# Kernel tuning notes

Measured on AMD Instinct MI355X. Metric: run time of the kernel, lower is better.

## Reference

```python
import jax, jax.numpy as jnp
import numpy as np

IN_SIZE = 1024
CLASSES = 7
N = 50000
LN_EPS = 1e-5


def _chain(x, w, b, g, beta):
    # Linear -> (Dropout=identity at eval) -> LayerNorm -> GELU(exact erf)
    h = x @ w.T + b
    mu = jnp.mean(h, axis=-1, keepdims=True)
    var = jnp.var(h, axis=-1, keepdims=True)
    h = (h - mu) / jnp.sqrt(var + LN_EPS) * g + beta
    return jax.nn.gelu(h, approximate=False)


def setup_inputs() -> dict:
    key = jax.random.key(0)
    ks = jax.random.split(key, 16)
    d = IN_SIZE
    std = 1.0 / np.sqrt(d)
    inp = {
        "features": jax.random.normal(ks[0], (N, d), jnp.float32),
        "c": jax.random.normal(ks[1], (N, CLASSES), jnp.float32),
        "key_w": jax.random.uniform(ks[2], (d, d), jnp.float32, -std, std),
        "key_b": jax.random.uniform(ks[3], (d,), jnp.float32, -std, std),
        "key_g": jnp.ones((d,), jnp.float32),
        "key_beta": jnp.zeros((d,), jnp.float32),
        "query_w": jax.random.uniform(ks[4], (d, d), jnp.float32, -std, std),
        "query_b": jax.random.uniform(ks[5], (d,), jnp.float32, -std, std),
        "query_g": jnp.ones((d,), jnp.float32),
        "query_beta": jnp.zeros((d,), jnp.float32),
        "value_w": jax.random.uniform(ks[6], (d, d), jnp.float32, -std, std),
        "value_b": jax.random.uniform(ks[7], (d,), jnp.float32, -std, std),
        "value_g": jnp.ones((d,), jnp.float32),
        "value_beta": jnp.zeros((d,), jnp.float32),
        "head_w": jax.random.uniform(ks[8], (CLASSES, CLASSES, d), jnp.float32, -1.0 / np.sqrt(CLASSES * d), 1.0 / np.sqrt(CLASSES * d)),
        "head_b": jax.random.uniform(ks[9], (CLASSES,), jnp.float32, -1.0 / np.sqrt(CLASSES * d), 1.0 / np.sqrt(CLASSES * d)),
    }
    return inp


def reference(features, c, key_w, key_b, key_g, key_beta,
              query_w, query_b, query_g, query_beta,
              value_w, value_b, value_g, value_beta,
              head_w, head_b):
    K = _chain(features, key_w, key_b, key_g, key_beta)          # [N, d]
    V = _chain(K, value_w, value_b, value_g, value_beta)         # [N, d]
    Q = _chain(K, query_w, query_b, query_g, query_beta)         # [N, d]
    # critical (top-scoring) instance per class
    top_idx = jnp.argmax(c, axis=0)                              # [classes]
    m_feats = K[top_idx]                                         # [classes, d]
    q_max = _chain(m_feats, query_w, query_b, query_g, query_beta)  # [classes, d]
    A = Q @ q_max.T                                              # [N, classes]
    A = jax.nn.softmax(A / jnp.sqrt(jnp.float32(Q.shape[1])), axis=0)
    B = A.T @ V                                                  # [classes, d]
    # Conv1d(classes, classes, kernel_size=d) on [1, classes, d] -> full contraction
    C = jnp.einsum('ik,oik->o', B, head_w) + head_b              # [classes]
    C = C.reshape(1, -1)
    return (C, A, B.reshape(1, CLASSES, -1))
```

## Files before the change

### kernel.cpp

```cpp
#include <hip/hip_runtime.h>


typedef unsigned short u16;
typedef __attribute__((ext_vector_type(8))) short          bf16x8;
typedef __attribute__((ext_vector_type(8))) unsigned short u16x8;
typedef __attribute__((ext_vector_type(4))) unsigned short u16x4;
typedef __attribute__((ext_vector_type(4))) float          f32x4;

#define DDIM  1024
#define NROWS 50000
#define MP    50176
#define NCLS  7
#define MPD4  12544

__device__ __forceinline__ u16 f2bf(float f) {
  unsigned u = __float_as_uint(f);
  u = (u + 0x7FFFu + ((u >> 16) & 1u)) >> 16;
  return (u16)u;
}
__device__ __forceinline__ float bf2f(u16 h) {
  return __uint_as_float(((unsigned)h) << 16);
}
__device__ __forceinline__ float gelu(float x) {
  return 0.5f * x * (1.0f + erff(x * 0.70710678118654752f));
}

__device__ __forceinline__ void load16_lds(const u16* g, u16* l) {
  __builtin_amdgcn_global_load_lds(
      (const __attribute__((address_space(1))) unsigned int*)(const void*)g,
      (__attribute__((address_space(3))) unsigned int*)(void*)l, 16, 0, 0);
}

#define MFMA_(a, b, c) __builtin_amdgcn_mfma_f32_16x16x32_bf16(a, b, c, 0, 0, 0)

__global__ __launch_bounds__(256) void k_convw(const float* __restrict__ kw,
                                               const float* __restrict__ vw,
                                               const float* __restrict__ qw,
                                               u16* __restrict__ Wk,
                                               u16* __restrict__ Wvq) {
  const int w = blockIdx.x >> 7;
  const int b = blockIdx.x & 127;
  const float* src = (w == 0) ? kw : (w == 1) ? vw : qw;
  u16* dst = (w == 0) ? Wk : (Wvq + (size_t)(w - 1) * DDIM * DDIM);
  for (int i = b * 256 + threadIdx.x; i < DDIM * DDIM / 8; i += 128 * 256) {
    const float4* p = (const float4*)(src + (size_t)i * 8);
    float4 f0 = p[0], f1 = p[1];
    u16x8 o;
    o[0] = f2bf(f0.x); o[1] = f2bf(f0.y); o[2] = f2bf(f0.z); o[3] = f2bf(f0.w);
    o[4] = f2bf(f1.x); o[5] = f2bf(f1.y); o[6] = f2bf(f1.z); o[7] = f2bf(f1.w);
    *(u16x8*)(dst + (size_t)i * 8) = o;
  }
}

template<int AFP32>
__global__ __launch_bounds__(256) void k_gemm(const float* __restrict__ Af,
                                              const u16* __restrict__ Ab,
                                              const u16* __restrict__ B,
                                              u16* __restrict__ C,
                                              int lnn, int ldc) {
  __shared__ __align__(16) u16 As[128 * 32];
  __shared__ __align__(16) u16 Bs[128 * 32];
  const int tid  = threadIdx.x;
  const int lane = tid & 63;
  const int cpx = gridDim.x >> 3;
  const int v   = (blockIdx.x & 7) * cpx + (blockIdx.x >> 3);
  const int m0 = (v >> lnn) * 128;
  const int n0 = (v & ((1 << lnn) - 1)) * 128;
  const int wid = tid >> 6;
  const int wr = (wid >> 1) * 64;
  const int wc = (wid & 1) * 64;

  const int rA = tid >> 2;
  const int slotl = tid & 3;
  const int swz = (rA >> 1) & 3;
  const int cA = ((slotl ^ swz) << 3);
  const u16* Bp0 = B + (size_t)(n0 + rA) * DDIM + cA;
  const u16* Bp1 = Bp0 + (size_t)64 * DDIM;
  const u16* Ap0 = nullptr; const u16* Ap1 = nullptr;
  const float* Fp0 = nullptr; const float* Fp1 = nullptr;
  bool av0 = false, av1 = false;
  if (AFP32) {
    av0 = (m0 + rA) < NROWS;
    av1 = (m0 + rA + 64) < NROWS;
    Fp0 = Af + (size_t)(m0 + rA) * DDIM + slotl * 8;
    Fp1 = Fp0 + (size_t)64 * DDIM;
  } else {
    Ap0 = Ab + (size_t)(m0 + rA) * DDIM + cA;
    Ap1 = Ap0 + (size_t)64 * DDIM;
  }
  const int wbase = wid * 64;
  u16* AsD0 = &As[(wbase)       * 8];
  u16* AsD1 = &As[(wbase + 256) * 8];
  u16* BsD0 = &Bs[(wbase)       * 8];
  u16* BsD1 = &Bs[(wbase + 256) * 8];
  u16* AsW0 = &As[rA * 32 + cA];
  u16* AsW1 = &As[(rA + 64) * 32 + cA];

  f32x4 acc[4][4] = {};
  const int fr = lane & 15;
  const int T  = lane >> 4;

  for (int k0 = 0; k0 < DDIM; k0 += 32) {
    float4 fa0, fb0, fa1, fb1;
    if (AFP32) {
      if (av0) { fa0 = *(const float4*)(Fp0 + k0); fb0 = *(const float4*)(Fp0 + k0 + 4); }
      if (av1) { fa1 = *(const float4*)(Fp1 + k0); fb1 = *(const float4*)(Fp1 + k0 + 4); }
    }
    __syncthreads();
    if (AFP32) {
      u16x8 o0 = {0,0,0,0,0,0,0,0}, o1 = {0,0,0,0,0,0,0,0};
      if (av0) {
        o0[0]=f2bf(fa0.x); o0[1]=f2bf(fa0.y); o0[2]=f2bf(fa0.z); o0[3]=f2bf(fa0.w);
        o0[4]=f2bf(fb0.x); o0[5]=f2bf(fb0.y); o0[6]=f2bf(fb0.z); o0[7]=f2bf(fb0.w);
      }
      if (av1) {
        o1[0]=f2bf(fa1.x); o1[1]=f2bf(fa1.y); o1[2]=f2bf(fa1.z); o1[3]=f2bf(fa1.w);
        o1[4]=f2bf(fb1.x); o1[5]=f2bf(fb1.y); o1[6]=f2bf(fb1.z); o1[7]=f2bf(fb1.w);
      }
      *(u16x8*)AsW0 = o0;
      *(u16x8*)AsW1 = o1;
    } else {
      load16_lds(Ap0 + k0, AsD0);
      load16_lds(Ap1 + k0, AsD1);
    }
    load16_lds(Bp0 + k0, BsD0);
    load16_lds(Bp1 + k0, BsD1);
    __syncthreads();
    bf16x8 a[4], b[4];
#pragma unroll
    for (int i = 0; i < 4; ++i) {
      const int R = wr + i * 16 + fr;
      a[i] = *(const bf16x8*)&As[R * 32 + ((T ^ ((R >> 1) & 3)) << 3)];
    }
#pragma unroll
    for (int j = 0; j < 4; ++j) {
      const int R = wc + j * 16 + fr;
      b[j] = *(const bf16x8*)&Bs[R * 32 + ((T ^ ((R >> 1) & 3)) << 3)];
    }
#pragma unroll
    for (int i = 0; i < 4; ++i)
#pragma unroll
      for (int j = 0; j < 4; ++j)
        acc[i][j] = MFMA_(a[i], b[j], acc[i][j]);
  }

  const int orow = (lane >> 4) * 4;
  const int ocol = lane & 15;
#pragma unroll
  for (int i = 0; i < 4; ++i)
#pragma unroll
    for (int j = 0; j < 4; ++j) {
      const size_t base = (size_t)(m0 + wr + i * 16 + orow) * ldc + (n0 + wc + j * 16 + ocol);
#pragma unroll
      for (int r = 0; r < 4; ++r)
        C[base + (size_t)r * ldc] = f2bf(acc[i][j][r]);
    }
}

__global__ __launch_bounds__(512, 2) void k_gemm256(const u16* __restrict__ A,
                                                    const u16* __restrict__ Bw,
                                                    u16* __restrict__ C) {
  extern __shared__ __align__(16) u16 smem[];
  u16* Abase = smem;
  u16* Bbase = smem + 32768;
  const int tid  = threadIdx.x;
  const int lane = tid & 63;
  const int wid  = tid >> 6;
  const int wr = wid >> 2;
  const int wc = wid & 3;
  const int bh = wc >> 1;
  const int bl = (wc & 1) * 64;
  const int fr = lane & 15;
  const int T  = lane >> 4;
  const int v  = (blockIdx.x & 7) * 196 + (blockIdx.x >> 3);
  const int m0 = (v >> 3) * 256;
  const int n0 = (v & 7) * 256;

  f32x4 acc[8][4] = {};

#define STAGE_A(KT, BB) do {                                                   \
    _Pragma("unroll") for (int h_ = 0; h_ < 2; ++h_)                           \
      _Pragma("unroll") for (int l_ = 0; l_ < 2; ++l_) {                       \
        const int s_ = l_ * 512 + tid;                                         \
        const int r_ = s_ >> 3;                                                \
        const int c_ = (s_ & 7) ^ (r_ & 7);                                    \
        load16_lds(A + (size_t)(m0 + h_ * 128 + r_) * DDIM + (KT) * 64 + c_ * 8, \
                   Abase + ((BB) * 2 + h_) * 8192 + s_ * 8);                   \
      } } while (0)

#define STAGE_B(KT, BB) do {                                                   \
    _Pragma("unroll") for (int h_ = 0; h_ < 2; ++h_)                           \
      _Pragma("unroll") for (int l_ = 0; l_ < 2; ++l_) {                       \
        const int s_ = l_ * 512 + tid;                                         \
        const int r_ = s_ >> 3;                                                \
        const int c_ = (s_ & 7) ^ (r_ & 7);                                    \
        load16_lds(Bw + (size_t)(n0 + h_ * 128 + r_) * DDIM + (KT) * 64 + c_ * 8, \
                   Bbase + ((BB) * 2 + h_) * 8192 + s_ * 8);                   \
      } } while (0)

#define PHASE_A(p) do {                                                        \
    bf16x8 afr[4];                                                             \
    _Pragma("unroll") for (int ks = 0; ks < 2; ++ks)                           \
      _Pragma("unroll") for (int ii = 0; ii < 2; ++ii) {                       \
        const int R = ((p) * 2 + ii) * 16 + fr;                                \
        afr[ks * 2 + ii] = *(const bf16x8*)&Ap[R * 64 + (((ks * 4 + T) ^ (R & 7)) << 3)]; \
      }                                                                        \
    __builtin_amdgcn_s_setprio(1);                                             \
    _Pragma("unroll") for (int ks = 0; ks < 2; ++ks)                           \
      _Pragma("unroll") for (int ii = 0; ii < 2; ++ii)                         \
        _Pragma("unroll") for (int j = 0; j < 4; ++j)                          \
          acc[(p) * 2 + ii][j] = MFMA_(afr[ks * 2 + ii], bfr[ks * 4 + j],      \
                                       acc[(p) * 2 + ii][j]);                  \
    __builtin_amdgcn_s_setprio(0);                                             \
  } while (0)

#define BARP() asm volatile("s_barrier" ::: "memory")

  STAGE_A(0, 0);
  STAGE_B(0, 0);
  asm volatile("s_waitcnt vmcnt(0)\n\ts_barrier" ::: "memory");

  for (int kt = 0; kt < 16; ++kt) {
    const int b = kt & 1;
    const u16* Ap = Abase + (b * 2 + wr) * 8192;
    const u16* Bp = Bbase + (b * 2 + bh) * 8192;
    const bool st = kt < 15;
    bf16x8 bfr[8];
    if (st) STAGE_A(kt + 1, b ^ 1);
#pragma unroll
    for (int ks = 0; ks < 2; ++ks)
#pragma unroll
      for (int j = 0; j < 4; ++j) {
        const int R = bl + j * 16 + fr;
        bfr[ks * 4 + j] = *(const bf16x8*)&Bp[R * 64 + (((ks * 4 + T) ^ (R & 7)) << 3)];
      }
    PHASE_A(0);
    BARP();
    if (st) STAGE_B(kt + 1, b ^ 1);
    PHASE_A(1);
    BARP();
    PHASE_A(2);
    BARP();
    PHASE_A(3);
    if (st)
      asm volatile("s_waitcnt vmcnt(0) lgkmcnt(0)\n\ts_barrier" ::: "memory");
  }
#undef STAGE_A
#undef STAGE_B
#undef PHASE_A
#undef BARP

#pragma unroll
  for (int i = 0; i < 8; ++i)
#pragma unroll
    for (int j = 0; j < 4; ++j) {
      const size_t base = (size_t)(m0 + wr * 128 + i * 16 + T * 4) * 2048
                        + (n0 + wc * 64 + j * 16 + fr);
#pragma unroll
      for (int r = 0; r < 4; ++r)
        C[base + (size_t)r * 2048] = f2bf(acc[i][j][r]);
    }
}

__global__ __launch_bounds__(256) void k_ln_k(const u16* __restrict__ h,
                                              const float* __restrict__ bias,
                                              const float* __restrict__ g,
                                              const float* __restrict__ beta,
                                              u16* __restrict__ out) {
  const int lane = threadIdx.x & 63;
  const int row = blockIdx.x * 4 + (threadIdx.x >> 6);
  const int c0 = lane * 8;
  u16x8* op0 = (u16x8*)(out + (size_t)row * DDIM + c0);
  u16x8* op1 = (u16x8*)(out + (size_t)row * DDIM + 512 + c0);
  if (row >= NROWS) {
    u16x8 z = {0, 0, 0, 0, 0, 0, 0, 0};
    *op0 = z; *op1 = z;
    return;
  }
  u16x8 h0 = *(const u16x8*)(h + (size_t)row * DDIM + c0);
  u16x8 h1 = *(const u16x8*)(h + (size_t)row * DDIM + 512 + c0);
  float4 a0 = *(const float4*)(bias + c0), a1 = *(const float4*)(bias + c0 + 4);
  float4 a2 = *(const float4*)(bias + 512 + c0), a3 = *(const float4*)(bias + 512 + c0 + 4);
  const float ba[8] = {a0.x, a0.y, a0.z, a0.w, a1.x, a1.y, a1.z, a1.w};
  const float bb[8] = {a2.x, a2.y, a2.z, a2.w, a3.x, a3.y, a3.z, a3.w};
  float v0[8], v1[8];
  float s1 = 0.f, s2 = 0.f;
#pragma unroll
  for (int e = 0; e < 8; ++e) {
    v0[e] = bf2f(h0[e]) + ba[e];
    v1[e] = bf2f(h1[e]) + bb[e];
    s1 += v0[e] + v1[e];
    s2 += v0[e] * v0[e] + v1[e] * v1[e];
  }
#pragma unroll
  for (int m = 1; m < 64; m <<= 1) {
    s1 += __shfl_xor(s1, m, 64);
    s2 += __shfl_xor(s2, m, 64);
  }
  const float mu = s1 * (1.0f / 1024.0f);
  const float var = s2 * (1.0f / 1024.0f) - mu * mu;
  const float rs = rsqrtf(var + 1e-5f);
  float4 g0 = *(const float4*)(g + c0), g1 = *(const float4*)(g + c0 + 4);
  float4 g2 = *(const float4*)(g + 512 + c0), g3 = *(const float4*)(g + 512 + c0 + 4);
  float4 t0 = *(const float4*)(beta + c0), t1 = *(const float4*)(beta + c0 + 4);
  float4 t2 = *(const float4*)(beta + 512 + c0), t3 = *(const float4*)(beta + 512 + c0 + 4);
  const float ga[8] = {g0.x, g0.y, g0.z, g0.w, g1.x, g1.y, g1.z, g1.w};
  const float gb[8] = {g2.x, g2.y, g2.z, g2.w, g3.x, g3.y, g3.z, g3.w};
  const float ta[8] = {t0.x, t0.y, t0.z, t0.w, t1.x, t1.y, t1.z, t1.w};
  const float tb[8] = {t2.x, t2.y, t2.z, t2.w, t3.x, t3.y, t3.z, t3.w};
  u16x8 o0, o1;
#pragma unroll
  for (int e = 0; e < 8; ++e) {
    o0[e] = f2bf(gelu((v0[e] - mu) * rs * ga[e] + ta[e]));
    o1[e] = f2bf(gelu((v1[e] - mu) * rs * gb[e] + tb[e]));
  }
  *op0 = o0; *op1 = o1;
}

__global__ __launch_bounds__(64) void k_qmax2(const float* __restrict__ argv,
                                              const int* __restrict__ argi,
                                              const u16* __restrict__ hvq,
                                              const float* __restrict__ qb,
                                              const float* __restrict__ qg,
                                              const float* __restrict__ qbeta,
                                              u16* __restrict__ qm) {
  const int j = blockIdx.x;
  const int lane = threadIdx.x;
  float bv = -3.4e38f; int bi = 0x7fffffff;
  for (int p = lane; p < 128; p += 64) {
    const float v = argv[p * NCLS + j];
    const int   i = argi[p * NCLS + j];
    if (v > bv || (v == bv && i < bi)) { bv = v; bi = i; }
  }
#pragma unroll
  for (int m = 1; m < 64; m <<= 1) {
    const float ov = __shfl_xor(bv, m, 64);
    const int   oi = __shfl_xor(bi, m, 64);
    if (ov > bv || (ov == bv && oi < bi)) { bv = ov; bi = oi; }
  }
  const int row = bi;
  const int c0 = lane * 8;
  const u16* hp = hvq + (size_t)row * 2048 + DDIM;
  u16x8 h0 = *(const u16x8*)(hp + c0);
  u16x8 h1 = *(const u16x8*)(hp + 512 + c0);
  float v0[8], v1[8];
  float s1 = 0.f, s2 = 0.f;
#pragma unroll
  for (int e = 0; e < 8; ++e) {
    v0[e] = bf2f(h0[e]) + qb[c0 + e];
    v1[e] = bf2f(h1[e]) + qb[512 + c0 + e];
    s1 += v0[e] + v1[e];
    s2 += v0[e] * v0[e] + v1[e] * v1[e];
  }
#pragma unroll
  for (int m = 1; m < 64; m <<= 1) {
    s1 += __shfl_xor(s1, m, 64);
    s2 += __shfl_xor(s2, m, 64);
  }
  const float mu = s1 * (1.0f / 1024.0f);
  const float var = s2 * (1.0f / 1024.0f) - mu * mu;
  const float rs = rsqrtf(var + 1e-5f);
  u16x8 o0, o1;
#pragma unroll
  for (int e = 0; e < 8; ++e) {
    o0[e] = f2bf(gelu((v0[e] - mu) * rs * qg[c0 + e] + qbeta[c0 + e]));
    o1[e] = f2bf(gelu((v1[e] - mu) * rs * qg[512 + c0 + e] + qbeta[512 + c0 + e]));
  }
  *(u16x8*)(qm + (size_t)j * DDIM + c0) = o0;
  *(u16x8*)(qm + (size_t)j * DDIM + 512 + c0) = o1;
}

__global__ __launch_bounds__(256) void k_ln_vq(const u16* __restrict__ h,
                                               const float* __restrict__ v_b,
                                               const float* __restrict__ v_g,
                                               const float* __restrict__ v_beta,
                                               const float* __restrict__ q_b,
                                               const float* __restrict__ q_g,
                                               const float* __restrict__ q_beta,
                                               const u16* __restrict__ qm,
                                               u16* __restrict__ V,
                                               float* __restrict__ logits) {
  __shared__ __align__(16) u16 sqm[NCLS * DDIM];
  const int tid = threadIdx.x;
  const int lane = tid & 63;
  const int half = (blockIdx.x >= MPD4) ? 1 : 0;
  const int rb = half ? (blockIdx.x - MPD4) : blockIdx.x;
  const int row = rb * 4 + (tid >> 6);
  if (half) {
    for (int i = tid; i < NCLS * DDIM / 8; i += 256)
      *(u16x8*)&sqm[i * 8] = *(const u16x8*)&qm[i * 8];
    __syncthreads();
  }
  if (row >= NROWS) return;
  const float* bias = half ? q_b : v_b;
  const float* gain = half ? q_g : v_g;
  const float* bet  = half ? q_beta : v_beta;
  const int c0 = lane * 8;
  const u16* hp = h + (size_t)row * 2048 + (size_t)half * DDIM;
  u16x8 h0 = *(const u16x8*)(hp + c0);
  u16x8 h1 = *(const u16x8*)(hp + 512 + c0);
  float4 a0 = *(const float4*)(bias + c0), a1 = *(const float4*)(bias + c0 + 4);
  float4 a2 = *(const float4*)(bias + 512 + c0), a3 = *(const float4*)(bias + 512 + c0 + 4);
  const float ba[8] = {a0.x, a0.y, a0.z, a0.w, a1.x, a1.y, a1.z, a1.w};
  const float bb[8] = {a2.x, a2.y, a2.z, a2.w, a3.x, a3.y, a3.z, a3.w};
  float v0[8], v1[8];
  float s1 = 0.f, s2 = 0.f;
#pragma unroll
  for (int e = 0; e < 8; ++e) {
    v0[e] = bf2f(h0[e]) + ba[e];
    v1[e] = bf2f(h1[e]) + bb[e];
    s1 += v0[e] + v1[e];
    s2 += v0[e] * v0[e] + v1[e] * v1[e];
  }
#pragma unroll
  for (int m = 1; m < 64; m <<= 1) {
    s1 += __shfl_xor(s1, m, 64);
    s2 += __shfl_xor(s2, m, 64);
  }
  const float mu = s1 * (1.0f / 1024.0f);
  const float var = s2 * (1.0f / 1024.0f) - mu * mu;
  const float rs = rsqrtf(var + 1e-5f);
  float4 g0 = *(const float4*)(gain + c0), g1 = *(const float4*)(gain + c0 + 4);
  float4 g2 = *(const float4*)(gain + 512 + c0), g3 = *(const float4*)(gain + 512 + c0 + 4);
  float4 t0 = *(const float4*)(bet + c0), t1 = *(const float4*)(bet + c0 + 4);
  float4 t2 = *(const float4*)(bet + 512 + c0), t3 = *(const float4*)(bet + 512 + c0 + 4);
  const float ga[8] = {g0.x, g0.y, g0.z, g0.w, g1.x, g1.y, g1.z, g1.w};
  const float gb[8] = {g2.x, g2.y, g2.z, g2.w, g3.x, g3.y, g3.z, g3.w};
  const float ta[8] = {t0.x, t0.y, t0.z, t0.w, t1.x, t1.y, t1.z, t1.w};
  const float tb[8] = {t2.x, t2.y, t2.z, t2.w, t3.x, t3.y, t3.z, t3.w};
  float y0[8], y1[8];
#pragma unroll
  for (int e = 0; e < 8; ++e) {
    y0[e] = gelu((v0[e] - mu) * rs * ga[e] + ta[e]);
    y1[e] = gelu((v1[e] - mu) * rs * gb[e] + tb[e]);
  }
  if (half == 0) {
    u16x8 o0, o1;
#pragma unroll
    for (int e = 0; e < 8; ++e) { o0[e] = f2bf(y0[e]); o1[e] = f2bf(y1[e]); }
    *(u16x8*)(V + (size_t)row * DDIM + c0) = o0;
    *(u16x8*)(V + (size_t)row * DDIM + 512 + c0) = o1;
  } else {
#pragma unroll
    for (int j = 0; j < NCLS; ++j) {
      u16x8 m0 = *(const u16x8*)&sqm[j * DDIM + c0];
      u16x8 m1 = *(const u16x8*)&sqm[j * DDIM + 512 + c0];
      float p = 0.f;
#pragma unroll
      for (int e = 0; e < 8; ++e) p += y0[e] * bf2f(m0[e]) + y1[e] * bf2f(m1[e]);
#pragma unroll
      for (int m = 1; m < 64; m <<= 1) p += __shfl_xor(p, m, 64);
      if (lane == 0) logits[(size_t)row * NCLS + j] = p * 0.03125f;
    }
  }
}

__global__ __launch_bounds__(256) void k_arg1(const float* __restrict__ c,
                                              float* __restrict__ pv,
                                              int* __restrict__ pi) {
  __shared__ float sv[256 * NCLS];
  __shared__ int   si[256 * NCLS];
  const int t = threadIdx.x;
  float bv[NCLS]; int bi[NCLS];
#pragma unroll
  for (int j = 0; j < NCLS; ++j) { bv[j] = -3.4e38f; bi[j] = 0x7fffffff; }
  for (int n = blockIdx.x * 256 + t; n < NROWS; n += 128 * 256) {
#pragma unroll
    for (int j = 0; j < NCLS; ++j) {
      const float v = c[(size_t)n * NCLS + j];
      if (v > bv[j]) { bv[j] = v; bi[j] = n; }
    }
  }
#pragma unroll
  for (int j = 0; j < NCLS; ++j) { sv[t * NCLS + j] = bv[j]; si[t * NCLS + j] = bi[j]; }
  __syncthreads();
  for (int s = 128; s > 0; s >>= 1) {
    if (t < s) {
#pragma unroll
      for (int j = 0; j < NCLS; ++j) {
        const float v2 = sv[(t + s) * NCLS + j]; const int i2 = si[(t + s) * NCLS + j];
        const float v1 = sv[t * NCLS + j];       const int i1 = si[t * NCLS + j];
        if (v2 > v1 || (v2 == v1 && i2 < i1)) { sv[t * NCLS + j] = v2; si[t * NCLS + j] = i2; }
      }
    }
    __syncthreads();
  }
  if (t < NCLS) { pv[blockIdx.x * NCLS + t] = sv[t]; pi[blockIdx.x * NCLS + t] = si[t]; }
}

__global__ __launch_bounds__(256) void k_softpart(const float* __restrict__ logits,
                                                  float* __restrict__ Pm,
                                                  float* __restrict__ Ps) {
  __shared__ float sm[256 * NCLS];
  const int t = threadIdx.x;
  float m[NCLS];
#pragma unroll
  for (int j = 0; j < NCLS; ++j) m[j] = -3.4e38f;
  for (int n = blockIdx.x * 256 + t; n < NROWS; n += 128 * 256)
#pragma unroll
    for (int j = 0; j < NCLS; ++j) m[j] = fmaxf(m[j], logits[(size_t)n * NCLS + j]);
#pragma unroll
  for (int j = 0; j < NCLS; ++j) sm[t * NCLS + j] = m[j];
  __syncthreads();
  for (int s = 128; s > 0; s >>= 1) {
    if (t < s)
#pragma unroll
      for (int j = 0; j < NCLS; ++j)
        sm[t * NCLS + j] = fmaxf(sm[t * NCLS + j], sm[(t + s) * NCLS + j]);
    __syncthreads();
  }
  float mloc[NCLS];
#pragma unroll
  for (int j = 0; j < NCLS; ++j) mloc[j] = sm[j];
  __syncthreads();
  float s[NCLS];
#pragma unroll
  for (int j = 0; j < NCLS; ++j) s[j] = 0.f;
  for (int n = blockIdx.x * 256 + t; n < NROWS; n += 128 * 256)
#pragma unroll
    for (int j = 0; j < NCLS; ++j) s[j] += expf(logits[(size_t)n * NCLS + j] - mloc[j]);
#pragma unroll
  for (int j = 0; j < NCLS; ++j) sm[t * NCLS + j] = s[j];
  __syncthreads();
  for (int st = 128; st > 0; st >>= 1) {
    if (t < st)
#pragma unroll
      for (int j = 0; j < NCLS; ++j) sm[t * NCLS + j] += sm[(t + st) * NCLS + j];
    __syncthreads();
  }
  if (t < NCLS) { Pm[blockIdx.x * NCLS + t] = mloc[t]; Ps[blockIdx.x * NCLS + t] = sm[t]; }
}

__global__ __launch_bounds__(256) void k_bpart(const float* __restrict__ logits,
                                               const float* __restrict__ Pm,
                                               const float* __restrict__ Ps,
                                               const u16* __restrict__ V,
                                               float* __restrict__ Aout,
                                               float* __restrict__ Pb) {
  __shared__ float sA[98 * NCLS];
  __shared__ float sM[NCLS], sR[NCLS];
  const int t = threadIdx.x;
  if (t < NCLS) {
    float M = -3.4e38f;
    for (int b = 0; b < 128; ++b) M = fmaxf(M, Pm[b * NCLS + t]);
    float S = 0.f;
    for (int b = 0; b < 128; ++b) S += Ps[b * NCLS + t] * expf(Pm[b * NCLS + t] - M);
    sM[t] = M; sR[t] = 1.0f / S;
  }
  __syncthreads();
  const int n0 = blockIdx.x * 98;
  int cnt = NROWS - n0;
  cnt = cnt < 0 ? 0 : (cnt > 98 ? 98 : cnt);
  for (int idx = t; idx < cnt * NCLS; idx += 256) {
    const int j = idx % NCLS;
    const float a = expf(logits[(size_t)n0 * NCLS + idx] - sM[j]) * sR[j];
    sA[idx] = a;
    Aout[(size_t)n0 * NCLS + idx] = a;
  }
  __syncthreads();
  float acc[NCLS][4] = {};
  for (int r = 0; r < cnt; ++r) {
    u16x4 vv = *(const u16x4*)&V[(size_t)(n0 + r) * DDIM + t * 4];
    const float f0 = bf2f(vv[0]), f1 = bf2f(vv[1]), f2 = bf2f(vv[2]), f3 = bf2f(vv[3]);
#pragma unroll
    for (int j = 0; j < NCLS; ++j) {
      const float a = sA[r * NCLS + j];
      acc[j][0] += a * f0; acc[j][1] += a * f1; acc[j][2] += a * f2; acc[j][3] += a * f3;
    }
  }
#pragma unroll
  for (int j = 0; j < NCLS; ++j) {
    f32x4 o = {acc[j][0], acc[j][1], acc[j][2], acc[j][3]};
    *(f32x4*)&Pb[((size_t)blockIdx.x * NCLS + j) * DDIM + t * 4] = o;
  }
}

__global__ void k_bred(const float* __restrict__ Pb, float* __restrict__ Bout) {
  const int idx = blockIdx.x * 256 + threadIdx.x;
  if (idx >= NCLS * DDIM) return;
  float s = 0.f;
  for (int p = 0; p < 512; ++p) s += Pb[(size_t)p * NCLS * DDIM + idx];
  Bout[idx] = s;
}

__global__ __launch_bounds__(256) void k_head(const float* __restrict__ Bmat,
                                              const float* __restrict__ hw,
                                              const float* __restrict__ hb,
                                              float* __restrict__ Cout) {
  const int o = blockIdx.x, t = threadIdx.x;
  float p = 0.f;
  for (int idx = t; idx < NCLS * DDIM; idx += 256)
    p += Bmat[idx] * hw[(size_t)o * NCLS * DDIM + idx];
#pragma unroll
  for (int m = 1; m < 64; m <<= 1) p += __shfl_xor(p, m, 64);
  __shared__ float w[4];
  if ((t & 63) == 0) w[t >> 6] = p;
  __syncthreads();
  if (t == 0) Cout[o] = w[0] + w[1] + w[2] + w[3] + hb[o];
}

extern "C" void kernel_launch(void* const* d_in, const int* in_sizes, int n_in,
                              void* d_out, int out_size, void* d_ws, size_t ws_size,
                              hipStream_t stream) {
  const float* features   = (const float*)d_in[0];
  const float* c_in       = (const float*)d_in[1];
  const float* key_w      = (const float*)d_in[2];
  const float* key_b      = (const float*)d_in[3];
  const float* key_g      = (const float*)d_in[4];
  const float* key_beta   = (const float*)d_in[5];
  const float* query_w    = (const float*)d_in[6];
  const float* query_b    = (const float*)d_in[7];
  const float* query_g    = (const float*)d_in[8];
  const float* query_beta = (const float*)d_in[9];
  const float* value_w    = (const float*)d_in[10];
  const float* value_b    = (const float*)d_in[11];
  const float* value_g    = (const float*)d_in[12];
  const float* value_beta = (const float*)d_in[13];
  const float* head_w     = (const float*)d_in[14];
  const float* head_b     = (const float*)d_in[15];

  char* ws = (char*)d_ws;
  const size_t SZB = (size_t)MP * DDIM * 2;
  u16* HbK  = (u16*)ws;
  u16* Kb   = (u16*)(ws + SZB);
  u16* HbVQ = (u16*)(ws + 2 * SZB);
  u16* Vb   = Kb;
  size_t off = 4 * SZB;
  u16* Wk  = (u16*)(ws + off); off += (size_t)DDIM * DDIM * 2;
  u16* Wvq = (u16*)(ws + off); off += (size_t)2 * DDIM * DDIM * 2;
  float* logits = (float*)(ws + off); off += ((size_t)NROWS * NCLS * 4 + 255) & ~(size_t)255;
  float* Pb  = (float*)(ws + off); off += (size_t)512 * NCLS * DDIM * 4;
  u16* qm    = (u16*)(ws + off); off += ((size_t)NCLS * DDIM * 2 + 255) & ~(size_t)255;
  float* Pmax = (float*)(ws + off); off += ((size_t)128 * NCLS * 4 + 255) & ~(size_t)255;
  float* Psum = (float*)(ws + off); off += ((size_t)128 * NCLS * 4 + 255) & ~(size_t)255;
  float* argv = (float*)(ws + off); off += ((size_t)128 * NCLS * 4 + 255) & ~(size_t)255;
  int*   argi = (int*)  (ws + off); off += ((size_t)128 * NCLS * 4 + 255) & ~(size_t)255;

  float* Cout = (float*)d_out;
  float* Aout = Cout + NCLS;
  float* Bout = Aout + (size_t)NROWS * NCLS;

  k_arg1<<<128, 256, 0, stream>>>(c_in, argv, argi);
  k_convw<<<384, 256, 0, stream>>>(key_w, value_w, query_w, Wk, Wvq);

  k_gemm<1><<<3136, 256, 0, stream>>>(features, nullptr, Wk, HbK, 3, 1024);
  k_ln_k<<<MPD4, 256, 0, stream>>>(HbK, key_b, key_g, key_beta, Kb);

  k_gemm256<<<1568, 512, 131072, stream>>>(Kb, Wvq, HbVQ);
  k_qmax2<<<NCLS, 64, 0, stream>>>(argv, argi, HbVQ, query_b, query_g, query_beta, qm);
  k_ln_vq<<<2 * MPD4, 256, 0, stream>>>(HbVQ, value_b, value_g, value_beta,
                                        query_b, query_g, query_beta, qm, Vb, logits);

  k_softpart<<<128, 256, 0, stream>>>(logits, Pmax, Psum);

  k_bpart<<<512, 256, 0, stream>>>(logits, Pmax, Psum, Vb, Aout, Pb);
  k_bred<<<28, 256, 0, stream>>>(Pb, Bout);
  k_head<<<NCLS, 256, 0, stream>>>(Bout, head_w, head_b, Cout);
}
```

Baseline: 726.7 us.

## Pre-convert features to bf16 and reuse 256-tile GEMM for key projection

Adds a standalone kernel that converts the fp32 features to a padded bf16 buffer, then runs the key projection through the larger 256x256 tiled, LDS-DMA pipelined GEMM instead of the 128-tile fp32-input GEMM that converted inline. The 256 GEMM is generalised with tile-count and leading-dimension parameters. The workspace is reshuffled so the VQ output reuses the converted-features buffer. This adds an extra pass over the features (fp32 read, bf16 write), traded for a faster main GEMM.

```diff
diff --git a/kernel.cpp b/kernel.cpp
--- a/kernel.cpp
+++ b/kernel.cpp
@@ -32,6 +32,25 @@
 }
 
 #define MFMA_(a, b, c) __builtin_amdgcn_mfma_f32_16x16x32_bf16(a, b, c, 0, 0, 0)
+
+__global__ __launch_bounds__(256) void k_convert(const float* __restrict__ src,
+                                                 u16* __restrict__ dst,
+                                                 int rows_total, int rows_valid) {
+  const size_t total = (size_t)rows_total * DDIM / 8;
+  const size_t stride = (size_t)gridDim.x * blockDim.x;
+  for (size_t i = (size_t)blockIdx.x * blockDim.x + threadIdx.x; i < total; i += stride) {
+    const size_t e = i * 8;
+    const int row = (int)(e >> 10);
+    u16x8 o = {0, 0, 0, 0, 0, 0, 0, 0};
+    if (row < rows_valid) {
+      const float4* p = (const float4*)(src + e);
+      float4 f0 = p[0], f1 = p[1];
+      o[0] = f2bf(f0.x); o[1] = f2bf(f0.y); o[2] = f2bf(f0.z); o[3] = f2bf(f0.w);
+      o[4] = f2bf(f1.x); o[5] = f2bf(f1.y); o[6] = f2bf(f1.z); o[7] = f2bf(f1.w);
+    }
+    *(u16x8*)(dst + e) = o;
+  }
+}
 
 __global__ __launch_bounds__(256) void k_convw(const float* __restrict__ kw,
                                                const float* __restrict__ vw,
@@ -52,114 +71,10 @@
   }
 }
 
-template<int AFP32>
-__global__ __launch_bounds__(256) void k_gemm(const float* __restrict__ Af,
-                                              const u16* __restrict__ Ab,
-                                              const u16* __restrict__ B,
-                                              u16* __restrict__ C,
-                                              int lnn, int ldc) {
-  __shared__ __align__(16) u16 As[128 * 32];
-  __shared__ __align__(16) u16 Bs[128 * 32];
-  const int tid  = threadIdx.x;
-  const int lane = tid & 63;
-  const int cpx = gridDim.x >> 3;
-  const int v   = (blockIdx.x & 7) * cpx + (blockIdx.x >> 3);
-  const int m0 = (v >> lnn) * 128;
-  const int n0 = (v & ((1 << lnn) - 1)) * 128;
-  const int wid = tid >> 6;
-  const int wr = (wid >> 1) * 64;
-  const int wc = (wid & 1) * 64;
-
-  const int rA = tid >> 2;
-  const int slotl = tid & 3;
-  const int swz = (rA >> 1) & 3;
-  const int cA = ((slotl ^ swz) << 3);
-  const u16* Bp0 = B + (size_t)(n0 + rA) * DDIM + cA;
-  const u16* Bp1 = Bp0 + (size_t)64 * DDIM;
-  const u16* Ap0 = nullptr; const u16* Ap1 = nullptr;
-  const float* Fp0 = nullptr; const float* Fp1 = nullptr;
-  bool av0 = false, av1 = false;
-  if (AFP32) {
-    av0 = (m0 + rA) < NROWS;
-    av1 = (m0 + rA + 64) < NROWS;
-    Fp0 = Af + (size_t)(m0 + rA) * DDIM + slotl * 8;
-    Fp1 = Fp0 + (size_t)64 * DDIM;
-  } else {
-    Ap0 = Ab + (size_t)(m0 + rA) * DDIM + cA;
-    Ap1 = Ap0 + (size_t)64 * DDIM;
-  }
-  const int wbase = wid * 64;
-  u16* AsD0 = &As[(wbase)       * 8];
-  u16* AsD1 = &As[(wbase + 256) * 8];
-  u16* BsD0 = &Bs[(wbase)       * 8];
-  u16* BsD1 = &Bs[(wbase + 256) * 8];
-  u16* AsW0 = &As[rA * 32 + cA];
-  u16* AsW1 = &As[(rA + 64) * 32 + cA];
-
-  f32x4 acc[4][4] = {};
-  const int fr = lane & 15;
-  const int T  = lane >> 4;
-
-  for (int k0 = 0; k0 < DDIM; k0 += 32) {
-    float4 fa0, fb0, fa1, fb1;
-    if (AFP32) {
-      if (av0) { fa0 = *(const float4*)(Fp0 + k0); fb0 = *(const float4*)(Fp0 + k0 + 4); }
-      if (av1) { fa1 = *(const float4*)(Fp1 + k0); fb1 = *(const float4*)(Fp1 + k0 + 4); }
-    }
-    __syncthreads();
-    if (AFP32) {
-      u16x8 o0 = {0,0,0,0,0,0,0,0}, o1 = {0,0,0,0,0,0,0,0};
-      if (av0) {
-        o0[0]=f2bf(fa0.x); o0[1]=f2bf(fa0.y); o0[2]=f2bf(fa0.z); o0[3]=f2bf(fa0.w);
-        o0[4]=f2bf(fb0.x); o0[5]=f2bf(fb0.y); o0[6]=f2bf(fb0.z); o0[7]=f2bf(fb0.w);
-      }
-      if (av1) {
-        o1[0]=f2bf(fa1.x); o1[1]=f2bf(fa1.y); o1[2]=f2bf(fa1.z); o1[3]=f2bf(fa1.w);
-        o1[4]=f2bf(fb1.x); o1[5]=f2bf(fb1.y); o1[6]=f2bf(fb1.z); o1[7]=f2bf(fb1.w);
-      }
-      *(u16x8*)AsW0 = o0;
-      *(u16x8*)AsW1 = o1;
-    } else {
-      load16_lds(Ap0 + k0, AsD0);
-      load16_lds(Ap1 + k0, AsD1);
-    }
-    load16_lds(Bp0 + k0, BsD0);
-    load16_lds(Bp1 + k0, BsD1);
-    __syncthreads();
-    bf16x8 a[4], b[4];
-#pragma unroll
-    for (int i = 0; i < 4; ++i) {
-      const int R = wr + i * 16 + fr;
-      a[i] = *(const bf16x8*)&As[R * 32 + ((T ^ ((R >> 1) & 3)) << 3)];
-    }
-#pragma unroll
-    for (int j = 0; j < 4; ++j) {
-      const int R = wc + j * 16 + fr;
-      b[j] = *(const bf16x8*)&Bs[R * 32 + ((T ^ ((R >> 1) & 3)) << 3)];
-    }
-#pragma unroll
-    for (int i = 0; i < 4; ++i)
-#pragma unroll
-      for (int j = 0; j < 4; ++j)
-        acc[i][j] = MFMA_(a[i], b[j], acc[i][j]);
-  }
-
-  const int orow = (lane >> 4) * 4;
-  const int ocol = lane & 15;
-#pragma unroll
-  for (int i = 0; i < 4; ++i)
-#pragma unroll
-    for (int j = 0; j < 4; ++j) {
-      const size_t base = (size_t)(m0 + wr + i * 16 + orow) * ldc + (n0 + wc + j * 16 + ocol);
-#pragma unroll
-      for (int r = 0; r < 4; ++r)
-        C[base + (size_t)r * ldc] = f2bf(acc[i][j][r]);
-    }
-}
-
 __global__ __launch_bounds__(512, 2) void k_gemm256(const u16* __restrict__ A,
                                                     const u16* __restrict__ Bw,
-                                                    u16* __restrict__ C) {
+                                                    u16* __restrict__ C,
+                                                    int lnn, int ldc) {
   extern __shared__ __align__(16) u16 smem[];
   u16* Abase = smem;
   u16* Bbase = smem + 32768;
@@ -172,9 +87,10 @@
   const int bl = (wc & 1) * 64;
   const int fr = lane & 15;
   const int T  = lane >> 4;
-  const int v  = (blockIdx.x & 7) * 196 + (blockIdx.x >> 3);
-  const int m0 = (v >> 3) * 256;
-  const int n0 = (v & 7) * 256;
+  const int cpx = gridDim.x >> 3;
+  const int v  = (blockIdx.x & 7) * cpx + (blockIdx.x >> 3);
+  const int m0 = (v >> lnn) * 256;
+  const int n0 = (v & ((1 << lnn) - 1)) * 256;
 
   f32x4 acc[8][4] = {};
 
@@ -254,11 +170,11 @@
   for (int i = 0; i < 8; ++i)
 #pragma unroll
     for (int j = 0; j < 4; ++j) {
-      const size_t base = (size_t)(m0 + wr * 128 + i * 16 + T * 4) * 2048
+      const size_t base = (size_t)(m0 + wr * 128 + i * 16 + T * 4) * ldc
                         + (n0 + wc * 64 + j * 16 + fr);
 #pragma unroll
       for (int r = 0; r < 4; ++r)
-        C[base + (size_t)r * 2048] = f2bf(acc[i][j][r]);
+        C[base + (size_t)r * ldc] = f2bf(acc[i][j][r]);
     }
 }
 
@@ -621,11 +537,12 @@
 
   char* ws = (char*)d_ws;
   const size_t SZB = (size_t)MP * DDIM * 2;
-  u16* HbK  = (u16*)ws;
-  u16* Kb   = (u16*)(ws + SZB);
-  u16* HbVQ = (u16*)(ws + 2 * SZB);
+  u16* Xb   = (u16*)ws;
+  u16* HbK  = (u16*)(ws + SZB);
+  u16* HbVQ = Xb;
+  u16* Kb   = (u16*)(ws + 2 * SZB);
   u16* Vb   = Kb;
-  size_t off = 4 * SZB;
+  size_t off = 3 * SZB;
   u16* Wk  = (u16*)(ws + off); off += (size_t)DDIM * DDIM * 2;
   u16* Wvq = (u16*)(ws + off); off += (size_t)2 * DDIM * DDIM * 2;
   float* logits = (float*)(ws + off); off += ((size_t)NROWS * NCLS * 4 + 255) & ~(size_t)255;
@@ -642,11 +559,12 @@
 
   k_arg1<<<128, 256, 0, stream>>>(c_in, argv, argi);
   k_convw<<<384, 256, 0, stream>>>(key_w, value_w, query_w, Wk, Wvq);
-
-  k_gemm<1><<<3136, 256, 0, stream>>>(features, nullptr, Wk, HbK, 3, 1024);
+  k_convert<<<2048, 256, 0, stream>>>(features, Xb, MP, NROWS);
+
+  k_gemm256<<<784, 512, 131072, stream>>>(Xb, Wk, HbK, 2, 1024);
   k_ln_k<<<MPD4, 256, 0, stream>>>(HbK, key_b, key_g, key_beta, Kb);
 
-  k_gemm256<<<1568, 512, 131072, stream>>>(Kb, Wvq, HbVQ);
+  k_gemm256<<<1568, 512, 131072, stream>>>(Kb, Wvq, HbVQ, 3, 2048);
   k_qmax2<<<NCLS, 64, 0, stream>>>(argv, argi, HbVQ, query_b, query_g, query_beta, qm);
   k_ln_vq<<<2 * MPD4, 256, 0, stream>>>(HbVQ, value_b, value_g, value_beta,
                                         query_b, query_g, query_beta, qm, Vb, logits);
```

Result: faster. 678.1 us (-6.7%).
